# Kernel optimization log

Hardware: AMD Instinct MI355X
Metric: run time of the kernel (lower is better)

## Reference

```python
import jax, jax.numpy as jnp
import numpy as np

EMBED_DIM = 2048
NUM_HEADS = 16
HEAD_DIM = EMBED_DIM // NUM_HEADS
SCALE = EMBED_DIM ** -0.5  # NOTE: original uses full embed_dim, not head_dim


def setup_inputs() -> dict:
    key = jax.random.key(0)
    ks = jax.random.split(key, 9)
    d = EMBED_DIM
    s = 1.0 / np.sqrt(d)
    inp = {
        "x": jax.random.normal(ks[0], (2, 2048, d), dtype=jnp.float32),
        "wq": jax.random.uniform(ks[1], (d, d), jnp.float32, -s, s),
        "bq": jnp.zeros((d,), jnp.float32),
        "wk": jax.random.uniform(ks[2], (d, d), jnp.float32, -s, s),
        "bk": jnp.zeros((d,), jnp.float32),
        "wv": jax.random.uniform(ks[3], (d, d), jnp.float32, -s, s),
        "bv": jnp.zeros((d,), jnp.float32),
        "wo": jax.random.uniform(ks[4], (d, d), jnp.float32, -s, s),
        "bo": jnp.zeros((d,), jnp.float32),
    }
    return inp


def reference(x, wq, bq, wk, bk, wv, bv, wo, bo):
    b, t, d = x.shape
    h, hd = NUM_HEADS, HEAD_DIM
    # projections (torch Linear: x @ W.T + b; here weights stored as [in, out])
    q = (x @ wq + bq).reshape(b, t, h, hd).transpose(0, 2, 1, 3)  # [b,h,t,hd]
    k = (x @ wk + bk).reshape(b, t, h, hd).transpose(0, 2, 1, 3)
    v = (x @ wv + bv).reshape(b, t, h, hd).transpose(0, 2, 1, 3)
    scores = jnp.einsum("bhqd,bhkd->bhqk", q, k) * SCALE
    probs = jax.nn.softmax(scores, axis=-1)
    attn = jnp.einsum("bhqk,bhkd->bhqd", probs, v)
    attn = attn.transpose(0, 2, 1, 3).reshape(b, t, d)
    return attn @ wo + bo
```

## Files before the change

kernel.cpp:

```cpp
#include <hip/hip_runtime.h>

typedef unsigned int u32;
typedef __bf16 bf16;
typedef bf16 bf16x2 __attribute__((ext_vector_type(2)));
typedef bf16 bf16x4 __attribute__((ext_vector_type(4)));
typedef bf16 bf16x8 __attribute__((ext_vector_type(8)));
typedef float f32x4 __attribute__((ext_vector_type(4)));
typedef float f32x16 __attribute__((ext_vector_type(16)));
typedef u32 u32x4 __attribute__((ext_vector_type(4)));

#define T_ 2048
#define D_ 2048
#define H_ 16
#define HD_ 128
#define SCALE_ 0.022097086912079608f
#define LOG2E_ 1.4426950408889634f

typedef __attribute__((address_space(1))) u32 gu32;
typedef __attribute__((address_space(3))) u32 lu32;

__device__ __forceinline__ void gload_lds16(const void* g, void* l) {
  __builtin_amdgcn_global_load_lds((gu32*)(void*)g, (lu32*)l, 16, 0, 0);
}

__device__ __forceinline__ u32 packbf(float a, float b) {
  union { bf16x2 v; u32 u; } c;
  c.v.x = (bf16)a; c.v.y = (bf16)b;
  return c.u;
}

__global__ void prep_kernel(const float* __restrict__ x, bf16* __restrict__ xb,
                            const float* __restrict__ w0, const float* __restrict__ w1,
                            const float* __restrict__ w2, const float* __restrict__ w3,
                            bf16* __restrict__ o0, bf16* __restrict__ o1,
                            bf16* __restrict__ o2, bf16* __restrict__ o3) {
  int z = blockIdx.z;
  int t = threadIdx.x;
  if (z == 4) {
    int b2 = blockIdx.y * 32 + blockIdx.x;
#pragma unroll
    for (int j = 0; j < 8; j++) {
      int i = b2 * 2048 + j * 256 + t;
      float4 v = ((const float4*)x)[i];
      bf16x4 o;
      o.x = (bf16)v.x; o.y = (bf16)v.y; o.z = (bf16)v.z; o.w = (bf16)v.w;
      ((bf16x4*)xb)[i] = o;
    }
    return;
  }
  const float* W = (z == 0) ? w0 : (z == 1) ? w1 : (z == 2) ? w2 : w3;
  bf16* O = (z == 0) ? o0 : (z == 1) ? o1 : (z == 2) ? o2 : o3;
  __shared__ float tile[64][65];
  int tx = t & 15, ty = t >> 4;
  int n0 = blockIdx.x * 64, k0 = blockIdx.y * 64;
#pragma unroll
  for (int i = 0; i < 4; i++) {
    float4 v = *(const float4*)&W[(size_t)(k0 + ty + i * 16) * D_ + n0 + tx * 4];
    tile[ty + i * 16][tx * 4 + 0] = v.x;
    tile[ty + i * 16][tx * 4 + 1] = v.y;
    tile[ty + i * 16][tx * 4 + 2] = v.z;
    tile[ty + i * 16][tx * 4 + 3] = v.w;
  }
  __syncthreads();
#pragma unroll
  for (int i = 0; i < 4; i++) {
    int n = ty + i * 16;
    bf16x4 o;
    o.x = (bf16)tile[tx * 4 + 0][n];
    o.y = (bf16)tile[tx * 4 + 1][n];
    o.z = (bf16)tile[tx * 4 + 2][n];
    o.w = (bf16)tile[tx * 4 + 3][n];
    *(bf16x4*)&O[(size_t)(n0 + n) * D_ + k0 + tx * 4] = o;
  }
}

__device__ __forceinline__ void stage_tile(const bf16* __restrict__ A,
                                           const bf16* __restrict__ Bt,
                                           char* aT, char* bT,
                                           int m0, int n0, int k0, int t) {
#pragma unroll
  for (int i = 0; i < 4; i++) {
    int L = i * 4096 + t * 16;
    int row = L >> 7;
    int kb = (L & 127) ^ ((row & 7) << 4);
    gload_lds16(A + (size_t)(m0 + row) * 2048 + k0 + (kb >> 1), aT + L);
    gload_lds16(Bt + (size_t)(n0 + row) * 2048 + k0 + (kb >> 1), bT + L);
  }
}

__device__ __forceinline__ void gemm_compute64(const char* aT, const char* bT,
                                               f32x4 acc[4][4], int lane, int wr, int wc) {
#pragma unroll
  for (int kk = 0; kk < 2; kk++) {
    int ak = kk * 64 + ((lane >> 4) << 4);
    bf16x8 af[4], bfv[4];
#pragma unroll
    for (int f = 0; f < 4; f++) {
      int ar = wr * 64 + f * 16 + (lane & 15);
      af[f] = *(const bf16x8*)(aT + ar * 128 + (ak ^ ((ar & 7) << 4)));
      int br = wc * 64 + f * 16 + (lane & 15);
      bfv[f] = *(const bf16x8*)(bT + br * 128 + (ak ^ ((br & 7) << 4)));
    }
#pragma unroll
    for (int mi = 0; mi < 4; mi++)
#pragma unroll
      for (int ni = 0; ni < 4; ni++)
        acc[mi][ni] = __builtin_amdgcn_mfma_f32_16x16x32_bf16(af[mi], bfv[ni], acc[mi][ni], 0, 0, 0);
  }
}

__device__ __forceinline__ void gemm_core_128(const bf16* __restrict__ A,
                                              const bf16* __restrict__ Bt,
                                              f32x4 acc[4][4], int m0, int n0) {
  __shared__ char smem[65536];
  const int t = threadIdx.x;
  const int lane = t & 63;
  const int wr = (t >> 7) & 1;
  const int wc = (t >> 6) & 1;
  stage_tile(A, Bt, smem, smem + 16384, m0, n0, 0, t);
  __syncthreads();
  int cur = 0;
  for (int k0 = 64; k0 < 2048; k0 += 64) {
    char* base = smem + (cur ^ 1) * 32768;
    stage_tile(A, Bt, base, base + 16384, m0, n0, k0, t);
    char* cbase = smem + cur * 32768;
    gemm_compute64(cbase, cbase + 16384, acc, lane, wr, wc);
    __syncthreads();
    cur ^= 1;
  }
  char* cbase = smem + cur * 32768;
  gemm_compute64(cbase, cbase + 16384, acc, lane, wr, wc);
}

__global__ __launch_bounds__(256, 2) void qkv_gemm_kernel(
    const bf16* __restrict__ xb,
    const bf16* __restrict__ wqt, const bf16* __restrict__ wkt, const bf16* __restrict__ wvt,
    const float* __restrict__ bq, const float* __restrict__ bk, const float* __restrict__ bv,
    bf16* __restrict__ Qb, bf16* __restrict__ Kb, bf16* __restrict__ Vtb) {
  const bf16* Bt; const float* bias; float scale;
  int z = blockIdx.z;
  if (z == 0)      { Bt = wqt; bias = bq; scale = SCALE_ * LOG2E_; }
  else if (z == 1) { Bt = wkt; bias = bk; scale = 1.0f; }
  else             { Bt = wvt; bias = bv; scale = 1.0f; }
  int bid = blockIdx.x;
  int wid = (bid & 7) * 64 + (bid >> 3);
  int n0 = (wid & 15) * 128, m0 = (wid >> 4) * 128;
  f32x4 zero = {0.f, 0.f, 0.f, 0.f};
  f32x4 acc[4][4];
#pragma unroll
  for (int mi = 0; mi < 4; mi++)
#pragma unroll
    for (int ni = 0; ni < 4; ni++) acc[mi][ni] = zero;
  gemm_core_128(xb, Bt, acc, m0, n0);
  int lane = threadIdx.x & 63;
  int wr = (threadIdx.x >> 7) & 1, wc = (threadIdx.x >> 6) & 1;
  if (z < 2) {
    bf16* Out = (z == 0) ? Qb : Kb;
#pragma unroll
    for (int ni = 0; ni < 4; ni++) {
      int cn = n0 + wc * 64 + ni * 16 + (lane & 15);
      float bb = bias[cn];
      int h = cn >> 7, hd = cn & 127;
#pragma unroll
      for (int mi = 0; mi < 4; mi++) {
        int rm = m0 + wr * 64 + mi * 16 + ((lane >> 4) << 2);
#pragma unroll
        for (int r = 0; r < 4; r++) {
          int mg = rm + r;
          int b = mg >> 11, tt = mg & 2047;
          Out[(size_t)((b * H_ + h) * T_ + tt) * HD_ + hd] = (bf16)((acc[mi][ni][r] + bb) * scale);
        }
      }
    }
  } else {
#pragma unroll
    for (int ni = 0; ni < 4; ni++) {
      int cn = n0 + wc * 64 + ni * 16 + (lane & 15);
      float bb = bias[cn];
      int h = cn >> 7, hd = cn & 127;
#pragma unroll
      for (int mi = 0; mi < 4; mi++) {
        int rm = m0 + wr * 64 + mi * 16 + ((lane >> 4) << 2);
        int b = rm >> 11, tt = rm & 2047;
        bf16x4 st;
        st.x = (bf16)(acc[mi][ni][0] + bb);
        st.y = (bf16)(acc[mi][ni][1] + bb);
        st.z = (bf16)(acc[mi][ni][2] + bb);
        st.w = (bf16)(acc[mi][ni][3] + bb);
        *(bf16x4*)&Vtb[((size_t)(b * H_ + h) * HD_ + hd) * T_ + tt] = st;
      }
    }
  }
}

__global__ __launch_bounds__(256, 2) void attn_kernel(
    const bf16* __restrict__ Qb, const bf16* __restrict__ Kb,
    const bf16* __restrict__ Vtb, bf16* __restrict__ Ab) {
  __shared__ char smem[65536];
  const int t = threadIdx.x, lane = t & 63, w = t >> 6;
  const int h0 = lane >> 5;
  const int q = lane & 31;
  int bid = blockIdx.x;
  int wid = (bid & 7) * 64 + (bid >> 3);
  const int bh = wid >> 4;
  const int q0 = (wid & 15) * 128;
  const bf16* Qh = Qb + (size_t)bh * T_ * HD_;
  const bf16* Kh = Kb + (size_t)bh * T_ * HD_;
  const bf16* Vh = Vtb + (size_t)bh * HD_ * T_;

  int soff[8];
#pragma unroll
  for (int kf = 0; kf < 8; kf++) soff[kf] = (kf * 32 + h0 * 16) ^ ((q & 7) << 4);
  const int kbase = q * 256;
  const int vbase = q * 128;

  bf16x8 qf[8];
  {
    const bf16* qrow = Qh + (size_t)(q0 + w * 32 + q) * HD_ + h0 * 8;
#pragma unroll
    for (int kf = 0; kf < 8; kf++) qf[kf] = *(const bf16x8*)(qrow + kf * 16);
  }

  f32x16 o[4];
#pragma unroll
  for (int nb = 0; nb < 4; nb++)
#pragma unroll
    for (int r = 0; r < 16; r++) o[nb][r] = 0.f;
  float m = -1e30f, l = 0.f;

  auto stage = [&](int kt, char* Kl, char* Vl) {
#pragma unroll
    for (int i = 0; i < 4; i++) {
      int L = i * 4096 + t * 16;
      int rowK = L >> 8;
      int kbK = (L & 255) ^ ((rowK & 7) << 4);
      gload_lds16(Kh + (size_t)(kt + rowK) * HD_ + (kbK >> 1), Kl + L);
      int rowV = L >> 7;
      int kbV = (L & 127) ^ ((rowV & 7) << 4);
      gload_lds16(Vh + (size_t)rowV * T_ + kt + (kbV >> 1), Vl + L);
    }
  };

  stage(0, smem, smem + 16384);
  __syncthreads();
  int cur = 0;

  for (int kt = 0; kt < T_; kt += 64) {
    const char* Klds = smem + cur * 32768;
    const char* Vlds = Klds + 16384;
    if (kt + 64 < T_) {
      char* nxt = smem + (cur ^ 1) * 32768;
      stage(kt + 64, nxt, nxt + 16384);
    }

    f32x16 s[2];
#pragma unroll
    for (int sub = 0; sub < 2; sub++)
#pragma unroll
      for (int r = 0; r < 16; r++) s[sub][r] = 0.f;
    __builtin_amdgcn_s_setprio(1);
#pragma unroll
    for (int kf = 0; kf < 8; kf++) {
#pragma unroll
      for (int sub = 0; sub < 2; sub++) {
        bf16x8 kfr = *(const bf16x8*)(Klds + kbase + sub * 8192 + soff[kf]);
        s[sub] = __builtin_amdgcn_mfma_f32_32x32x16_bf16(kfr, qf[kf], s[sub], 0, 0, 0);
      }
    }
    __builtin_amdgcn_s_setprio(0);

    float mx = fmaxf(s[0][0], s[0][1]);
#pragma unroll
    for (int sub = 0; sub < 2; sub++)
#pragma unroll
      for (int r = (sub == 0 ? 2 : 0); r < 16; r += 2)
        mx = fmaxf(mx, fmaxf(s[sub][r], s[sub][r + 1]));
    mx = fmaxf(mx, __shfl_xor(mx, 32));
    if (__any(mx > m + 8.f)) {
      float mn = fmaxf(m, mx);
      float fac = exp2f(m - mn);
      m = mn;
      l *= fac;
#pragma unroll
      for (int nb = 0; nb < 4; nb++)
#pragma unroll
        for (int r = 0; r < 16; r++) o[nb][r] *= fac;
    }
    float rs = 0.f;
#pragma unroll
    for (int sub = 0; sub < 2; sub++)
#pragma unroll
      for (int r = 0; r < 16; r++) {
        float p = exp2f(s[sub][r] - m);
        s[sub][r] = p;
        rs += p;
      }
    rs += __shfl_xor(rs, 32);
    l += rs;

    bf16x8 pfrag[4];
#pragma unroll
    for (int sub = 0; sub < 2; sub++) {
#pragma unroll
      for (int c = 0; c < 2; c++) {
        u32 X0 = packbf(s[sub][8 * c + 0], s[sub][8 * c + 1]);
        u32 X1 = packbf(s[sub][8 * c + 2], s[sub][8 * c + 3]);
        u32 Y0 = packbf(s[sub][8 * c + 4], s[sub][8 * c + 5]);
        u32 Y1 = packbf(s[sub][8 * c + 6], s[sub][8 * c + 7]);
        u32 sX0 = (u32)__shfl_xor((int)X0, 32);
        u32 sX1 = (u32)__shfl_xor((int)X1, 32);
        u32 sY0 = (u32)__shfl_xor((int)Y0, 32);
        u32 sY1 = (u32)__shfl_xor((int)Y1, 32);
        u32x4 wv;
        wv.x = h0 ? sY0 : X0;
        wv.y = h0 ? sY1 : X1;
        wv.z = h0 ? Y0 : sX0;
        wv.w = h0 ? Y1 : sX1;
        union { u32x4 u; bf16x8 b; } cv;
        cv.u = wv;
        pfrag[sub * 2 + c] = cv.b;
      }
    }

    __builtin_amdgcn_s_setprio(1);
#pragma unroll
    for (int nb = 0; nb < 4; nb++) {
#pragma unroll
      for (int ks = 0; ks < 4; ks++) {
        bf16x8 vf = *(const bf16x8*)(Vlds + vbase + nb * 4096 + soff[ks]);
        o[nb] = __builtin_amdgcn_mfma_f32_32x32x16_bf16(vf, pfrag[ks], o[nb], 0, 0, 0);
      }
    }
    __builtin_amdgcn_s_setprio(0);
    __syncthreads();
    cur ^= 1;
  }

  float inv = 1.f / l;
  int b = bh >> 4, hh = bh & 15;
  bf16* orow = Ab + ((size_t)b * T_ + q0 + w * 32 + q) * D_ + hh * HD_;
#pragma unroll
  for (int nb = 0; nb < 4; nb++)
#pragma unroll
    for (int g = 0; g < 4; g++) {
      bf16x4 st;
      st.x = (bf16)(o[nb][4 * g + 0] * inv);
      st.y = (bf16)(o[nb][4 * g + 1] * inv);
      st.z = (bf16)(o[nb][4 * g + 2] * inv);
      st.w = (bf16)(o[nb][4 * g + 3] * inv);
      *(bf16x4*)(orow + nb * 32 + 8 * g + 4 * h0) = st;
    }
}

__global__ __launch_bounds__(256, 2) void out_gemm_kernel(
    const bf16* __restrict__ Ab, const bf16* __restrict__ wot,
    const float* __restrict__ bo, float* __restrict__ out) {
  int bid = blockIdx.x;
  int wid = (bid & 7) * 64 + (bid >> 3);
  int n0 = (wid & 15) * 128, m0 = (wid >> 4) * 128;
  f32x4 zero = {0.f, 0.f, 0.f, 0.f};
  f32x4 acc[4][4];
#pragma unroll
  for (int mi = 0; mi < 4; mi++)
#pragma unroll
    for (int ni = 0; ni < 4; ni++) acc[mi][ni] = zero;
  gemm_core_128(Ab, wot, acc, m0, n0);
  int lane = threadIdx.x & 63;
  int wr = (threadIdx.x >> 7) & 1, wc = (threadIdx.x >> 6) & 1;
#pragma unroll
  for (int ni = 0; ni < 4; ni++) {
    int cn = n0 + wc * 64 + ni * 16 + (lane & 15);
    float bb = bo[cn];
#pragma unroll
    for (int mi = 0; mi < 4; mi++) {
      int rm = m0 + wr * 64 + mi * 16 + ((lane >> 4) << 2);
#pragma unroll
      for (int r = 0; r < 4; r++)
        out[(size_t)(rm + r) * D_ + cn] = acc[mi][ni][r] + bb;
    }
  }
}

extern "C" void kernel_launch(void* const* d_in, const int* in_sizes, int n_in,
                              void* d_out, int out_size, void* d_ws, size_t ws_size,
                              hipStream_t stream) {
  const float* x  = (const float*)d_in[0];
  const float* wq = (const float*)d_in[1];
  const float* bq = (const float*)d_in[2];
  const float* wk = (const float*)d_in[3];
  const float* bk = (const float*)d_in[4];
  const float* wv = (const float*)d_in[5];
  const float* bv = (const float*)d_in[6];
  const float* wo = (const float*)d_in[7];
  const float* bo = (const float*)d_in[8];
  float* out = (float*)d_out;
  char* ws = (char*)d_ws;

  bf16* xb  = (bf16*)(ws);
  bf16* wqt = (bf16*)(ws + 16777216);
  bf16* wkt = (bf16*)(ws + 25165824);
  bf16* wvt = (bf16*)(ws + 33554432);
  bf16* wot = (bf16*)(ws + 41943040);
  bf16* Qb  = (bf16*)(ws + 50331648);
  bf16* Kb  = (bf16*)(ws + 67108864);
  bf16* Vtb = (bf16*)(ws + 83886080);
  bf16* Ab  = xb;

  prep_kernel<<<dim3(32, 32, 5), 256, 0, stream>>>(x, xb, wq, wk, wv, wo, wqt, wkt, wvt, wot);
  qkv_gemm_kernel<<<dim3(512, 1, 3), 256, 0, stream>>>(xb, wqt, wkt, wvt, bq, bk, bv, Qb, Kb, Vtb);
  attn_kernel<<<512, 256, 0, stream>>>(Qb, Kb, Vtb, Ab);
  out_gemm_kernel<<<512, 256, 0, stream>>>(Ab, wot, bo, out);

  (void)in_sizes; (void)n_in; (void)out_size; (void)ws_size;
}
```

Measured before the change: 384.5 us.

## Enlarge GEMM tiles to 128x256 with 8 warps and explicit vmcnt pipelining

The QKV and output GEMMs now use 512-thread blocks computing 128x256 tiles, so each A tile is reused across twice as many columns. Loads run through a two-stage LDS buffer (96 KB) with manual s_waitcnt/s_barrier control in place of __syncthreads. The attention kernel drops its s_setprio hints and precomputed LDS offsets, computing addresses inline and using a simpler max reduction. The larger LDS footprint and 512 threads per block may cut occupancy, and two blocks of 96 KB may not fit per CU.

```diff
diff --git a/kernel.cpp b/kernel.cpp
--- a/kernel.cpp
+++ b/kernel.cpp
@@ -74,65 +74,77 @@
   }
 }
 
-__device__ __forceinline__ void stage_tile(const bf16* __restrict__ A,
-                                           const bf16* __restrict__ Bt,
-                                           char* aT, char* bT,
-                                           int m0, int n0, int k0, int t) {
-#pragma unroll
-  for (int i = 0; i < 4; i++) {
-    int L = i * 4096 + t * 16;
+
+__device__ __forceinline__ void stage3(const bf16* __restrict__ A,
+                                       const bf16* __restrict__ Bt,
+                                       char* buf, int m0, int n0, int k0, int t) {
+#pragma unroll
+  for (int i = 0; i < 2; i++) {
+    int L = i * 8192 + t * 16;
     int row = L >> 7;
     int kb = (L & 127) ^ ((row & 7) << 4);
-    gload_lds16(A + (size_t)(m0 + row) * 2048 + k0 + (kb >> 1), aT + L);
-    gload_lds16(Bt + (size_t)(n0 + row) * 2048 + k0 + (kb >> 1), bT + L);
-  }
-}
-
-__device__ __forceinline__ void gemm_compute64(const char* aT, const char* bT,
-                                               f32x4 acc[4][4], int lane, int wr, int wc) {
-#pragma unroll
-  for (int kk = 0; kk < 2; kk++) {
-    int ak = kk * 64 + ((lane >> 4) << 4);
-    bf16x8 af[4], bfv[4];
-#pragma unroll
-    for (int f = 0; f < 4; f++) {
-      int ar = wr * 64 + f * 16 + (lane & 15);
-      af[f] = *(const bf16x8*)(aT + ar * 128 + (ak ^ ((ar & 7) << 4)));
-      int br = wc * 64 + f * 16 + (lane & 15);
-      bfv[f] = *(const bf16x8*)(bT + br * 128 + (ak ^ ((br & 7) << 4)));
-    }
-#pragma unroll
-    for (int mi = 0; mi < 4; mi++)
-#pragma unroll
-      for (int ni = 0; ni < 4; ni++)
-        acc[mi][ni] = __builtin_amdgcn_mfma_f32_16x16x32_bf16(af[mi], bfv[ni], acc[mi][ni], 0, 0, 0);
-  }
-}
-
-__device__ __forceinline__ void gemm_core_128(const bf16* __restrict__ A,
+    gload_lds16(A + (size_t)(m0 + row) * 2048 + k0 + (kb >> 1), buf + L);
+  }
+#pragma unroll
+  for (int i = 0; i < 4; i++) {
+    int L = i * 8192 + t * 16;
+    int row = L >> 7;
+    int kb = (L & 127) ^ ((row & 7) << 4);
+    gload_lds16(Bt + (size_t)(n0 + row) * 2048 + k0 + (kb >> 1), buf + 16384 + L);
+  }
+}
+
+__device__ __forceinline__ void phase16(const char* buf, f32x4 acc[4][4],
+                                        int kk, int lane, int wr, int wc) {
+  const char* aT = buf;
+  const char* bT = buf + 16384;
+  int ak = kk * 64 + ((lane >> 4) << 4);
+  bf16x8 af[4], bfv[4];
+#pragma unroll
+  for (int f = 0; f < 4; f++) {
+    int ar = wr * 64 + f * 16 + (lane & 15);
+    af[f] = *(const bf16x8*)(aT + ar * 128 + (ak ^ ((ar & 7) << 4)));
+    int br = wc * 64 + f * 16 + (lane & 15);
+    bfv[f] = *(const bf16x8*)(bT + br * 128 + (ak ^ ((br & 7) << 4)));
+  }
+#pragma unroll
+  for (int mi = 0; mi < 4; mi++)
+#pragma unroll
+    for (int ni = 0; ni < 4; ni++)
+      acc[mi][ni] = __builtin_amdgcn_mfma_f32_16x16x32_bf16(af[mi], bfv[ni], acc[mi][ni], 0, 0, 0);
+}
+
+__device__ __forceinline__ void gemm_core_256(const bf16* __restrict__ A,
                                               const bf16* __restrict__ Bt,
                                               f32x4 acc[4][4], int m0, int n0) {
-  __shared__ char smem[65536];
+  __shared__ char smem[98304];
   const int t = threadIdx.x;
   const int lane = t & 63;
-  const int wr = (t >> 7) & 1;
-  const int wc = (t >> 6) & 1;
-  stage_tile(A, Bt, smem, smem + 16384, m0, n0, 0, t);
-  __syncthreads();
+  const int wid = t >> 6;
+  const int wr = wid >> 2, wc = wid & 3;
+  stage3(A, Bt, smem, m0, n0, 0, t);
+  stage3(A, Bt, smem + 49152, m0, n0, 64, t);
+  asm volatile("s_waitcnt vmcnt(6)" ::: "memory");
+  __builtin_amdgcn_s_barrier();
   int cur = 0;
-  for (int k0 = 64; k0 < 2048; k0 += 64) {
-    char* base = smem + (cur ^ 1) * 32768;
-    stage_tile(A, Bt, base, base + 16384, m0, n0, k0, t);
-    char* cbase = smem + cur * 32768;
-    gemm_compute64(cbase, cbase + 16384, acc, lane, wr, wc);
-    __syncthreads();
+#pragma unroll 1
+  for (int kt = 0; kt < 32; kt++) {
+    char* buf = smem + cur * 49152;
+    phase16(buf, acc, 0, lane, wr, wc);
+    phase16(buf, acc, 1, lane, wr, wc);
+    __builtin_amdgcn_s_barrier();
+    if (kt + 2 < 32) {
+      stage3(A, Bt, buf, m0, n0, (kt + 2) * 64, t);
+      asm volatile("s_waitcnt vmcnt(6)" ::: "memory");
+    } else {
+      asm volatile("s_waitcnt vmcnt(0)" ::: "memory");
+    }
+    __builtin_amdgcn_s_barrier();
     cur ^= 1;
   }
-  char* cbase = smem + cur * 32768;
-  gemm_compute64(cbase, cbase + 16384, acc, lane, wr, wc);
-}
-
-__global__ __launch_bounds__(256, 2) void qkv_gemm_kernel(
+}
+
+__global__ __launch_bounds__(512, 2) void qkv_gemm_kernel(
     const bf16* __restrict__ xb,
     const bf16* __restrict__ wqt, const bf16* __restrict__ wkt, const bf16* __restrict__ wvt,
     const float* __restrict__ bq, const float* __restrict__ bk, const float* __restrict__ bv,
@@ -143,17 +155,18 @@
   else if (z == 1) { Bt = wkt; bias = bk; scale = 1.0f; }
   else             { Bt = wvt; bias = bv; scale = 1.0f; }
   int bid = blockIdx.x;
-  int wid = (bid & 7) * 64 + (bid >> 3);
-  int n0 = (wid & 15) * 128, m0 = (wid >> 4) * 128;
+  int wid = (bid & 7) * 32 + (bid >> 3);
+  int m0 = (wid >> 3) * 128, n0 = (wid & 7) * 256;
   f32x4 zero = {0.f, 0.f, 0.f, 0.f};
   f32x4 acc[4][4];
 #pragma unroll
   for (int mi = 0; mi < 4; mi++)
 #pragma unroll
     for (int ni = 0; ni < 4; ni++) acc[mi][ni] = zero;
-  gemm_core_128(xb, Bt, acc, m0, n0);
+  gemm_core_256(xb, Bt, acc, m0, n0);
   int lane = threadIdx.x & 63;
-  int wr = (threadIdx.x >> 7) & 1, wc = (threadIdx.x >> 6) & 1;
+  int w8 = threadIdx.x >> 6;
+  int wr = w8 >> 2, wc = w8 & 3;
   if (z < 2) {
     bf16* Out = (z == 0) ? Qb : Kb;
 #pragma unroll
@@ -208,12 +221,6 @@
   const bf16* Kh = Kb + (size_t)bh * T_ * HD_;
   const bf16* Vh = Vtb + (size_t)bh * HD_ * T_;
 
-  int soff[8];
-#pragma unroll
-  for (int kf = 0; kf < 8; kf++) soff[kf] = (kf * 32 + h0 * 16) ^ ((q & 7) << 4);
-  const int kbase = q * 256;
-  const int vbase = q * 128;
-
   bf16x8 qf[8];
   {
     const bf16* qrow = Qh + (size_t)(q0 + w * 32 + q) * HD_ + h0 * 8;
@@ -258,23 +265,21 @@
     for (int sub = 0; sub < 2; sub++)
 #pragma unroll
       for (int r = 0; r < 16; r++) s[sub][r] = 0.f;
-    __builtin_amdgcn_s_setprio(1);
 #pragma unroll
     for (int kf = 0; kf < 8; kf++) {
 #pragma unroll
       for (int sub = 0; sub < 2; sub++) {
-        bf16x8 kfr = *(const bf16x8*)(Klds + kbase + sub * 8192 + soff[kf]);
+        int rr = sub * 32 + q;
+        bf16x8 kfr = *(const bf16x8*)(Klds + rr * 256 + ((kf * 32 + h0 * 16) ^ ((rr & 7) << 4)));
         s[sub] = __builtin_amdgcn_mfma_f32_32x32x16_bf16(kfr, qf[kf], s[sub], 0, 0, 0);
       }
     }
-    __builtin_amdgcn_s_setprio(0);
-
-    float mx = fmaxf(s[0][0], s[0][1]);
+
+    float mx = s[0][0];
 #pragma unroll
     for (int sub = 0; sub < 2; sub++)
 #pragma unroll
-      for (int r = (sub == 0 ? 2 : 0); r < 16; r += 2)
-        mx = fmaxf(mx, fmaxf(s[sub][r], s[sub][r + 1]));
+      for (int r = 0; r < 16; r++) mx = fmaxf(mx, s[sub][r]);
     mx = fmaxf(mx, __shfl_xor(mx, 32));
     if (__any(mx > m + 8.f)) {
       float mn = fmaxf(m, mx);
@@ -322,16 +327,15 @@
       }
     }
 
-    __builtin_amdgcn_s_setprio(1);
 #pragma unroll
     for (int nb = 0; nb < 4; nb++) {
+      int vr = nb * 32 + q;
 #pragma unroll
       for (int ks = 0; ks < 4; ks++) {
-        bf16x8 vf = *(const bf16x8*)(Vlds + vbase + nb * 4096 + soff[ks]);
+        bf16x8 vf = *(const bf16x8*)(Vlds + vr * 128 + ((ks * 32 + h0 * 16) ^ ((vr & 7) << 4)));
         o[nb] = __builtin_amdgcn_mfma_f32_32x32x16_bf16(vf, pfrag[ks], o[nb], 0, 0, 0);
       }
     }
-    __builtin_amdgcn_s_setprio(0);
     __syncthreads();
     cur ^= 1;
   }
@@ -352,21 +356,22 @@
     }
 }
 
-__global__ __launch_bounds__(256, 2) void out_gemm_kernel(
+__global__ __launch_bounds__(512, 2) void out_gemm_kernel(
     const bf16* __restrict__ Ab, const bf16* __restrict__ wot,
     const float* __restrict__ bo, float* __restrict__ out) {
   int bid = blockIdx.x;
-  int wid = (bid & 7) * 64 + (bid >> 3);
-  int n0 = (wid & 15) * 128, m0 = (wid >> 4) * 128;
+  int wid = (bid & 7) * 32 + (bid >> 3);
+  int m0 = (wid >> 3) * 128, n0 = (wid & 7) * 256;
   f32x4 zero = {0.f, 0.f, 0.f, 0.f};
   f32x4 acc[4][4];
 #pragma unroll
   for (int mi = 0; mi < 4; mi++)
 #pragma unroll
     for (int ni = 0; ni < 4; ni++) acc[mi][ni] = zero;
-  gemm_core_128(Ab, wot, acc, m0, n0);
+  gemm_core_256(Ab, wot, acc, m0, n0);
   int lane = threadIdx.x & 63;
-  int wr = (threadIdx.x >> 7) & 1, wc = (threadIdx.x >> 6) & 1;
+  int w8 = threadIdx.x >> 6;
+  int wr = w8 >> 2, wc = w8 & 3;
 #pragma unroll
   for (int ni = 0; ni < 4; ni++) {
     int cn = n0 + wc * 64 + ni * 16 + (lane & 15);
@@ -407,9 +412,9 @@
   bf16* Ab  = xb;
 
   prep_kernel<<<dim3(32, 32, 5), 256, 0, stream>>>(x, xb, wq, wk, wv, wo, wqt, wkt, wvt, wot);
-  qkv_gemm_kernel<<<dim3(512, 1, 3), 256, 0, stream>>>(xb, wqt, wkt, wvt, bq, bk, bv, Qb, Kb, Vtb);
+  qkv_gemm_kernel<<<dim3(256, 1, 3), 512, 0, stream>>>(xb, wqt, wkt, wvt, bq, bk, bv, Qb, Kb, Vtb);
   attn_kernel<<<512, 256, 0, stream>>>(Qb, Kb, Vtb, Ab);
-  out_gemm_kernel<<<512, 256, 0, stream>>>(Ab, wot, bo, out);
+  out_gemm_kernel<<<256, 512, 0, stream>>>(Ab, wot, bo, out);
 
   (void)in_sizes; (void)n_in; (void)out_size; (void)ws_size;
 }
```

Measured after the change: 391.3 us. About the same (+1.8%).
